# Optimization experiments

Measured on AMD Instinct MI355X. Metric: run time of the kernel, lower is better.

## Reference

```python
import jax, jax.numpy as jnp
import numpy as np


def _hausdorff(x, y):
    # x, y: [B, C, N, D] point sets per (batch, channel); rows are points.
    x2 = jnp.sum(x * x, axis=-1)                       # [B, C, N]
    y2 = jnp.sum(y * y, axis=-1)                       # [B, C, M]
    xy = jnp.einsum('bcnd,bcmd->bcnm', x, y)           # [B, C, N, M]
    d2 = x2[..., :, None] + y2[..., None, :] - 2.0 * xy
    d = jnp.sqrt(jnp.maximum(d2, 0.0))                 # Euclidean distances
    d_fwd = jnp.max(jnp.min(d, axis=-1), axis=-1)      # max_n min_m, [B, C]
    d_bwd = jnp.max(jnp.min(d, axis=-2), axis=-1)      # max_m min_n, [B, C]
    return jnp.maximum(d_fwd, d_bwd)                   # symmetric Hausdorff [B, C]


def setup_inputs() -> dict:
    key = jax.random.key(0)
    k1, k2 = jax.random.split(key)
    B, C, H, W = 8, 3, 1024, 1024
    inp = jax.random.normal(k1, (B, C, H, W), dtype=jnp.float32)
    tgt = jax.random.normal(k2, (B, C, H, W), dtype=jnp.float32)
    return {'input': inp, 'target': tgt}


def reference(input, target):
    h = _hausdorff(input, target)        # [B, C]
    # original: sum_i mean_c(h[i]) / B == mean over (B, C)
    return jnp.mean(h)
```

## Files before the change

### kernel.cpp

```cpp
#include <hip/hip_runtime.h>
#include <math.h>

constexpr int BC = 24;
constexpr int N  = 1024;
constexpr int D  = 1024;
constexpr int TILE = 128;
constexpr int SKF = 40;

typedef short short8 __attribute__((ext_vector_type(8)));
typedef float f32x4  __attribute__((ext_vector_type(4)));
typedef long lng2    __attribute__((ext_vector_type(2)));

#define FINF 3.402823466e+38f


__device__ inline unsigned pk_bf16(float a, float b) {
    unsigned ua = __float_as_uint(a) + 0x8000u;
    unsigned ub = __float_as_uint(b) + 0x8000u;
    return __builtin_amdgcn_perm(ub, ua, 0x07060302);
}

__device__ inline int pk_fp8x4(float a, float b, float c, float d) {
    int w = __builtin_amdgcn_cvt_pk_fp8_f32(a, b, 0, false);
    w = __builtin_amdgcn_cvt_pk_fp8_f32(c, d, w, true);
    return w;
}

__global__ __launch_bounds__(256) void prep_kernel(const float* __restrict__ X,
                                                   const float* __restrict__ Y,
                                                   unsigned char* __restrict__ Xf8,
                                                   unsigned char* __restrict__ Yf8,
                                                   float* __restrict__ xn,
                                                   float* __restrict__ yn) {
    int wave = threadIdx.x >> 6, lane = threadIdx.x & 63;
    int r16 = lane & 15, quad = lane >> 4;
    int wid = blockIdx.x * 4 + wave;

    float4 c0, c1, c2, c3;
    float4 n0, n1, n2, n3;

    auto src_of = [&](int st) -> const float* {
        bool isY = st >= 24576;
        int s = isY ? st - 24576 : s = st;
        s = isY ? st - 24576 : st;
        int bc = s >> 10, rkp = s & 1023;
        int R = rkp >> 4, Kp = rkp & 15;
        return (isY ? Y : X) + ((size_t)bc * N + R * 16 + r16) * D + Kp * 64 + quad * 8;
    };

    {
        const float* p = src_of(wid);
        c0 = *(const float4*)p;        c1 = *(const float4*)(p + 4);
        c2 = *(const float4*)(p + 32); c3 = *(const float4*)(p + 36);
    }
    #pragma unroll
    for (int it = 0; it < 4; it++) {
        int st = wid + it * 12288;
        if (it < 3) {
            const float* p = src_of(wid + (it + 1) * 12288);
            n0 = *(const float4*)p;        n1 = *(const float4*)(p + 4);
            n2 = *(const float4*)(p + 32); n3 = *(const float4*)(p + 36);
        }
        bool isY = st >= 24576;
        int s = isY ? st - 24576 : st;
        uint4 w;
        w.x = (unsigned)pk_fp8x4(c0.x, c0.y, c0.z, c0.w);
        w.y = (unsigned)pk_fp8x4(c1.x, c1.y, c1.z, c1.w);
        w.z = (unsigned)pk_fp8x4(c2.x, c2.y, c2.z, c2.w);
        w.w = (unsigned)pk_fp8x4(c3.x, c3.y, c3.z, c3.w);
        *(uint4*)((isY ? Yf8 : Xf8) + (size_t)s * 1024 + lane * 16) = w;

        float sm = c0.x*c0.x + c0.y*c0.y + c0.z*c0.z + c0.w*c0.w
                 + c1.x*c1.x + c1.y*c1.y + c1.z*c1.z + c1.w*c1.w
                 + c2.x*c2.x + c2.y*c2.y + c2.z*c2.z + c2.w*c2.w
                 + c3.x*c3.x + c3.y*c3.y + c3.z*c3.z + c3.w*c3.w;
        sm += __shfl_xor(sm, 16, 64);
        sm += __shfl_xor(sm, 32, 64);
        if (quad == 0) {
            int bc = s >> 10, R = (s & 1023) >> 4;
            atomicAdd(&(isY ? yn : xn)[bc * N + R * 16 + r16], sm);
        }
        c0 = n0; c1 = n1; c2 = n2; c3 = n3;
    }
}

__global__ __launch_bounds__(256, 3) void tile_f8_kernel(const unsigned char* __restrict__ Xf8,
                                                         const unsigned char* __restrict__ Yf8,
                                                         const float* __restrict__ xn,
                                                         const float* __restrict__ yn,
                                                         unsigned* __restrict__ rowmin,
                                                         unsigned* __restrict__ colmin) {
    int id = blockIdx.x;
    int bc = id >> 6;
    int tn = (id >> 3) & 7, tm = id & 7;

    int wave = threadIdx.x >> 6, lane = threadIdx.x & 63;
    int wr = wave >> 1, wc = wave & 1;
    int quad = lane >> 4, tx = lane & 15;

    const unsigned char* Xb = Xf8 + (size_t)bc * 1024 * 1024;
    const unsigned char* Yb = Yf8 + (size_t)bc * 1024 * 1024;
    const unsigned char* ax = Xb + (size_t)(tn * 8 + wr * 4) * 16 * 1024 + lane * 16;
    const unsigned char* by = Yb + (size_t)(tm * 8 + wc * 4) * 16 * 1024 + lane * 16;

    f32x4 acc[4][4];
    #pragma unroll
    for (int i = 0; i < 4; i++)
        #pragma unroll
        for (int j = 0; j < 4; j++) acc[i][j] = (f32x4)0.f;

    lng2 a[2][4], b[2][4];
    #pragma unroll
    for (int mi = 0; mi < 4; mi++) {
        a[0][mi] = *(const lng2*)(ax + mi * 16384);
        b[0][mi] = *(const lng2*)(by + mi * 16384);
    }
    #pragma unroll
    for (int Kp = 0; Kp < 16; Kp++) {
        int cur = Kp & 1, nxt = cur ^ 1;
        if (Kp < 15) {
            #pragma unroll
            for (int mi = 0; mi < 4; mi++) {
                a[nxt][mi] = *(const lng2*)(ax + mi * 16384 + (Kp + 1) * 1024);
                b[nxt][mi] = *(const lng2*)(by + mi * 16384 + (Kp + 1) * 1024);
            }
        }
        #pragma unroll
        for (int mi = 0; mi < 4; mi++)
            #pragma unroll
            for (int mj = 0; mj < 4; mj++)
                acc[mi][mj] = __builtin_amdgcn_mfma_f32_16x16x32_fp8_fp8(a[cur][mi].x, b[cur][mj].x, acc[mi][mj], 0, 0, 0);
        #pragma unroll
        for (int mi = 0; mi < 4; mi++)
            #pragma unroll
            for (int mj = 0; mj < 4; mj++)
                acc[mi][mj] = __builtin_amdgcn_mfma_f32_16x16x32_fp8_fp8(a[cur][mi].y, b[cur][mj].y, acc[mi][mj], 0, 0, 0);
    }

    int rbase = bc * N + tn * TILE + wr * 64;
    int cbase = bc * N + tm * TILE + wc * 64;
    float xnr[4][4], ynr[4];
    #pragma unroll
    for (int mi = 0; mi < 4; mi++)
        #pragma unroll
        for (int r = 0; r < 4; r++) xnr[mi][r] = xn[rbase + mi * 16 + quad * 4 + r];
    #pragma unroll
    for (int mj = 0; mj < 4; mj++) ynr[mj] = yn[cbase + mj * 16 + tx];

    float rmin[4][4], cmin[4];
    #pragma unroll
    for (int mi = 0; mi < 4; mi++)
        #pragma unroll
        for (int r = 0; r < 4; r++) rmin[mi][r] = FINF;
    #pragma unroll
    for (int mj = 0; mj < 4; mj++) cmin[mj] = FINF;

    #pragma unroll
    for (int mi = 0; mi < 4; mi++)
        #pragma unroll
        for (int mj = 0; mj < 4; mj++)
            #pragma unroll
            for (int r = 0; r < 4; r++) {
                float d2 = fmaxf(xnr[mi][r] + ynr[mj] - 2.f * acc[mi][mj][r], 0.f);
                rmin[mi][r] = fminf(rmin[mi][r], d2);
                cmin[mj]    = fminf(cmin[mj], d2);
            }

    #pragma unroll
    for (int m = 1; m < 16; m <<= 1)
        #pragma unroll
        for (int mi = 0; mi < 4; mi++)
            #pragma unroll
            for (int r = 0; r < 4; r++)
                rmin[mi][r] = fminf(rmin[mi][r], __shfl_xor(rmin[mi][r], m, 64));
    if (tx == 0) {
        #pragma unroll
        for (int mi = 0; mi < 4; mi++)
            #pragma unroll
            for (int r = 0; r < 4; r++)
                atomicMin(&rowmin[rbase + mi * 16 + quad * 4 + r], __float_as_uint(rmin[mi][r]));
    }
    #pragma unroll
    for (int m = 16; m < 64; m <<= 1)
        #pragma unroll
        for (int mj = 0; mj < 4; mj++)
            cmin[mj] = fminf(cmin[mj], __shfl_xor(cmin[mj], m, 64));
    if (quad == 0) {
        #pragma unroll
        for (int mj = 0; mj < 4; mj++)
            atomicMin(&colmin[cbase + mj * 16 + tx], __float_as_uint(cmin[mj]));
    }
}

__global__ __launch_bounds__(256) void norms_kernel(const float* __restrict__ X,
                                                    const float* __restrict__ Y,
                                                    float* __restrict__ xn,
                                                    float* __restrict__ yn) {
    int w = threadIdx.x >> 6, lane = threadIdx.x & 63;
    long rid = (long)blockIdx.x * 4 + w;
    bool isY = rid >= (long)BC * N;
    long row = isY ? rid - (long)BC * N : rid;
    const float* src = (isY ? Y : X) + row * D;
    float s = 0.f;
    #pragma unroll
    for (int q = 0; q < 4; q++) {
        float4 v = ((const float4*)src)[lane + q * 64];
        s += v.x * v.x + v.y * v.y + v.z * v.z + v.w * v.w;
    }
    #pragma unroll
    for (int m = 1; m < 64; m <<= 1) s += __shfl_xor(s, m, 64);
    if (lane == 0) (isY ? yn : xn)[row] = s;
}

__global__ __launch_bounds__(256) void tile_conv_kernel(const float* __restrict__ X,
                                                        const float* __restrict__ Y,
                                                        const float* __restrict__ xn,
                                                        const float* __restrict__ yn,
                                                        unsigned* __restrict__ rowmin,
                                                        unsigned* __restrict__ colmin) {
    __shared__ unsigned short Xs[TILE * SKF];
    __shared__ unsigned short Ys[TILE * SKF];
    int bc = blockIdx.z, tn = blockIdx.y, tm = blockIdx.x;
    const float* Xb = X + ((size_t)bc * N + (size_t)tn * TILE) * D;
    const float* Yb = Y + ((size_t)bc * N + (size_t)tm * TILE) * D;

    int t = threadIdx.x;
    int srow = t >> 3, sq = t & 7;
    int wave = t >> 6, lane = t & 63;
    int wr = wave >> 1, wc = wave & 1;
    int quad = lane >> 4, tx = lane & 15;

    f32x4 acc[4][4];
    #pragma unroll
    for (int i = 0; i < 4; i++)
        #pragma unroll
        for (int j = 0; j < 4; j++) acc[i][j] = (f32x4)0.f;

    float4 xv[4], yv[4];
    #pragma unroll
    for (int i = 0; i < 4; i++) {
        xv[i] = *(const float4*)(Xb + (size_t)(srow + i * 32) * D + sq * 4);
        yv[i] = *(const float4*)(Yb + (size_t)(srow + i * 32) * D + sq * 4);
    }

    for (int k0 = 0; k0 < D; k0 += 32) {
        __syncthreads();
        #pragma unroll
        for (int i = 0; i < 4; i++) {
            uint2 px; px.x = pk_bf16(xv[i].x, xv[i].y); px.y = pk_bf16(xv[i].z, xv[i].w);
            *(uint2*)&Xs[(srow + i * 32) * SKF + sq * 4] = px;
            uint2 py; py.x = pk_bf16(yv[i].x, yv[i].y); py.y = pk_bf16(yv[i].z, yv[i].w);
            *(uint2*)&Ys[(srow + i * 32) * SKF + sq * 4] = py;
        }
        __syncthreads();
        if (k0 + 32 < D) {
            #pragma unroll
            for (int i = 0; i < 4; i++) {
                xv[i] = *(const float4*)(Xb + (size_t)(srow + i * 32) * D + k0 + 32 + sq * 4);
                yv[i] = *(const float4*)(Yb + (size_t)(srow + i * 32) * D + k0 + 32 + sq * 4);
            }
        }
        short8 af[4], bg[4];
        #pragma unroll
        for (int mi = 0; mi < 4; mi++)
            af[mi] = *(const short8*)&Xs[(wr * 64 + mi * 16 + tx) * SKF + quad * 8];
        #pragma unroll
        for (int mj = 0; mj < 4; mj++)
            bg[mj] = *(const short8*)&Ys[(wc * 64 + mj * 16 + tx) * SKF + quad * 8];
        #pragma unroll
        for (int mi = 0; mi < 4; mi++)
            #pragma unroll
            for (int mj = 0; mj < 4; mj++)
                acc[mi][mj] = __builtin_amdgcn_mfma_f32_16x16x32_bf16(af[mi], bg[mj], acc[mi][mj], 0, 0, 0);
    }

    int rbase = bc * N + tn * TILE + wr * 64;
    int cbase = bc * N + tm * TILE + wc * 64;
    float xnr[4][4], ynr[4];
    #pragma unroll
    for (int mi = 0; mi < 4; mi++)
        #pragma unroll
        for (int r = 0; r < 4; r++) xnr[mi][r] = xn[rbase + mi * 16 + quad * 4 + r];
    #pragma unroll
    for (int mj = 0; mj < 4; mj++) ynr[mj] = yn[cbase + mj * 16 + tx];

    float rmin[4][4], cmin[4];
    #pragma unroll
    for (int mi = 0; mi < 4; mi++)
        #pragma unroll
        for (int r = 0; r < 4; r++) rmin[mi][r] = FINF;
    #pragma unroll
    for (int mj = 0; mj < 4; mj++) cmin[mj] = FINF;

    #pragma unroll
    for (int mi = 0; mi < 4; mi++)
        #pragma unroll
        for (int mj = 0; mj < 4; mj++)
            #pragma unroll
            for (int r = 0; r < 4; r++) {
                float d2 = fmaxf(xnr[mi][r] + ynr[mj] - 2.f * acc[mi][mj][r], 0.f);
                rmin[mi][r] = fminf(rmin[mi][r], d2);
                cmin[mj]    = fminf(cmin[mj], d2);
            }

    #pragma unroll
    for (int m = 1; m < 16; m <<= 1)
        #pragma unroll
        for (int mi = 0; mi < 4; mi++)
            #pragma unroll
            for (int r = 0; r < 4; r++)
                rmin[mi][r] = fminf(rmin[mi][r], __shfl_xor(rmin[mi][r], m, 64));
    if (tx == 0) {
        #pragma unroll
        for (int mi = 0; mi < 4; mi++)
            #pragma unroll
            for (int r = 0; r < 4; r++)
                atomicMin(&rowmin[rbase + mi * 16 + quad * 4 + r], __float_as_uint(rmin[mi][r]));
    }
    #pragma unroll
    for (int m = 16; m < 64; m <<= 1)
        #pragma unroll
        for (int mj = 0; mj < 4; mj++)
            cmin[mj] = fminf(cmin[mj], __shfl_xor(cmin[mj], m, 64));
    if (quad == 0) {
        #pragma unroll
        for (int mj = 0; mj < 4; mj++)
            atomicMin(&colmin[cbase + mj * 16 + tx], __float_as_uint(cmin[mj]));
    }
}

__global__ __launch_bounds__(256) void finalize_kernel(const unsigned* __restrict__ rowmin,
                                                       const unsigned* __restrict__ colmin,
                                                       float* __restrict__ out) {
    int bc = blockIdx.x;
    float v = 0.f;
    for (int i = threadIdx.x; i < N; i += 256) {
        v = fmaxf(v, __uint_as_float(rowmin[bc * N + i]));
        v = fmaxf(v, __uint_as_float(colmin[bc * N + i]));
    }
    #pragma unroll
    for (int m = 1; m < 64; m <<= 1) v = fmaxf(v, __shfl_xor(v, m, 64));
    __shared__ float ws[4];
    int lane = threadIdx.x & 63, w = threadIdx.x >> 6;
    if (lane == 0) ws[w] = v;
    __syncthreads();
    if (threadIdx.x == 0) {
        float m = fmaxf(fmaxf(ws[0], ws[1]), fmaxf(ws[2], ws[3]));
        atomicAdd(out, sqrtf(m) * (1.0f / (float)BC));
    }
}

extern "C" void kernel_launch(void* const* d_in, const int* in_sizes, int n_in,
                              void* d_out, int out_size, void* d_ws, size_t ws_size,
                              hipStream_t stream) {
    const float* X = (const float*)d_in[0];
    const float* Y = (const float*)d_in[1];
    float* out = (float*)d_out;

    unsigned* rowmin = (unsigned*)d_ws;
    unsigned* colmin = rowmin + BC * N;
    float* xn = (float*)(colmin + BC * N);
    float* yn = xn + BC * N;
    size_t head = (size_t)4 * BC * N * 4;
    size_t f8_bytes = (size_t)BC * N * D;

    hipMemsetAsync(d_ws, 0xFF, (size_t)2 * BC * N * 4, stream);
    hipMemsetAsync(xn, 0, (size_t)2 * BC * N * 4, stream);
    hipMemsetAsync(d_out, 0, sizeof(float), stream);

    if (ws_size >= head + 2 * f8_bytes) {
        unsigned char* Xf8 = (unsigned char*)d_ws + head;
        unsigned char* Yf8 = Xf8 + f8_bytes;
        prep_kernel<<<3072, 256, 0, stream>>>(X, Y, Xf8, Yf8, xn, yn);
        tile_f8_kernel<<<1536, 256, 0, stream>>>(Xf8, Yf8, xn, yn, rowmin, colmin);
    } else {
        dim3 grid(N / TILE, N / TILE, BC);
        norms_kernel<<<2 * BC * N / 4, 256, 0, stream>>>(X, Y, xn, yn);
        tile_conv_kernel<<<grid, 256, 0, stream>>>(X, Y, xn, yn, rowmin, colmin);
    }
    finalize_kernel<<<BC, 256, 0, stream>>>(rowmin, colmin, out);
}
```

Baseline: 270.0 us.

## Restructure fp8 prep kernel to whole-row waves with direct norm stores

The prep kernel now gives each wave eight full rows instead of strided 16x64 sub-tiles. Each lane reads contiguous float4s and writes fp8 bytes to the same swizzled layout through a computed inner offset. The row norm is reduced with a full-wave shuffle and stored directly, which removes the atomicAdds and the memset that zeroed the norm buffers. The grid is halved and a two-row-ahead register prefetch pipeline is used, at the cost of 4-byte scattered stores instead of 16-byte stores.

New measurement: 287.2 us. 6.4% more time.

```diff
diff --git a/kernel.cpp b/kernel.cpp
--- a/kernel.cpp
+++ b/kernel.cpp
@@ -33,54 +33,44 @@
                                                    float* __restrict__ xn,
                                                    float* __restrict__ yn) {
     int wave = threadIdx.x >> 6, lane = threadIdx.x & 63;
-    int r16 = lane & 15, quad = lane >> 4;
-    int wid = blockIdx.x * 4 + wave;
-
-    float4 c0, c1, c2, c3;
-    float4 n0, n1, n2, n3;
-
-    auto src_of = [&](int st) -> const float* {
-        bool isY = st >= 24576;
-        int s = isY ? st - 24576 : s = st;
-        s = isY ? st - 24576 : st;
-        int bc = s >> 10, rkp = s & 1023;
-        int R = rkp >> 4, Kp = rkp & 15;
-        return (isY ? Y : X) + ((size_t)bc * N + R * 16 + r16) * D + Kp * 64 + quad * 8;
-    };
-
-    {
-        const float* p = src_of(wid);
-        c0 = *(const float4*)p;        c1 = *(const float4*)(p + 4);
-        c2 = *(const float4*)(p + 32); c3 = *(const float4*)(p + 36);
-    }
-    #pragma unroll
-    for (int it = 0; it < 4; it++) {
-        int st = wid + it * 12288;
-        if (it < 3) {
-            const float* p = src_of(wid + (it + 1) * 12288);
-            n0 = *(const float4*)p;        n1 = *(const float4*)(p + 4);
-            n2 = *(const float4*)(p + 32); n3 = *(const float4*)(p + 36);
-        }
-        bool isY = st >= 24576;
-        int s = isY ? st - 24576 : st;
-        uint4 w;
-        w.x = (unsigned)pk_fp8x4(c0.x, c0.y, c0.z, c0.w);
-        w.y = (unsigned)pk_fp8x4(c1.x, c1.y, c1.z, c1.w);
-        w.z = (unsigned)pk_fp8x4(c2.x, c2.y, c2.z, c2.w);
-        w.w = (unsigned)pk_fp8x4(c3.x, c3.y, c3.z, c3.w);
-        *(uint4*)((isY ? Yf8 : Xf8) + (size_t)s * 1024 + lane * 16) = w;
-
-        float sm = c0.x*c0.x + c0.y*c0.y + c0.z*c0.z + c0.w*c0.w
-                 + c1.x*c1.x + c1.y*c1.y + c1.z*c1.z + c1.w*c1.w
-                 + c2.x*c2.x + c2.y*c2.y + c2.z*c2.z + c2.w*c2.w
-                 + c3.x*c3.x + c3.y*c3.y + c3.z*c3.z + c3.w*c3.w;
-        sm += __shfl_xor(sm, 16, 64);
-        sm += __shfl_xor(sm, 32, 64);
-        if (quad == 0) {
-            int bc = s >> 10, R = (s & 1023) >> 4;
-            atomicAdd(&(isY ? yn : xn)[bc * N + R * 16 + r16], sm);
-        }
-        c0 = n0; c1 = n1; c2 = n2; c3 = n3;
+    int rid0 = (blockIdx.x * 4 + wave) * 8;
+    bool isY = rid0 >= 24576;
+    int row0 = isY ? rid0 - 24576 : rid0;
+    const float* __restrict__ src = (isY ? Y : X) + (size_t)row0 * D + lane * 4;
+    unsigned char* __restrict__ dst = isY ? Yf8 : Xf8;
+    float* __restrict__ nrm = isY ? yn : xn;
+
+    int KpL   = lane >> 4;
+    int inner = (((lane >> 1) & 3) << 8) | (((lane >> 3) & 1) << 3) | ((lane & 1) << 2);
+    unsigned char* dbase = dst + (size_t)((row0 & ~15) + KpL) * 1024
+                               + (row0 & 15) * 16 + inner;
+
+    float4 A[4], Bv[4], Cv[4];
+    #pragma unroll
+    for (int q = 0; q < 4; q++) A[q]  = *(const float4*)(src + q * 256);
+    #pragma unroll
+    for (int q = 0; q < 4; q++) Bv[q] = *(const float4*)(src + D + q * 256);
+
+    #pragma unroll
+    for (int r = 0; r < 8; r++) {
+        if (r < 6) {
+            #pragma unroll
+            for (int q = 0; q < 4; q++)
+                Cv[q] = *(const float4*)(src + (size_t)(r + 2) * D + q * 256);
+        }
+        float s = 0.f;
+        #pragma unroll
+        for (int q = 0; q < 4; q++) {
+            unsigned w = (unsigned)pk_fp8x4(A[q].x, A[q].y, A[q].z, A[q].w);
+            *(unsigned*)(dbase + q * 4096 + r * 16) = w;
+            s += A[q].x * A[q].x + A[q].y * A[q].y
+               + A[q].z * A[q].z + A[q].w * A[q].w;
+        }
+        #pragma unroll
+        for (int m = 1; m < 64; m <<= 1) s += __shfl_xor(s, m, 64);
+        if (lane == 0) nrm[row0 + r] = s;
+        #pragma unroll
+        for (int q = 0; q < 4; q++) { A[q] = Bv[q]; Bv[q] = Cv[q]; }
     }
 }
 
@@ -365,13 +355,12 @@
     size_t f8_bytes = (size_t)BC * N * D;
 
     hipMemsetAsync(d_ws, 0xFF, (size_t)2 * BC * N * 4, stream);
-    hipMemsetAsync(xn, 0, (size_t)2 * BC * N * 4, stream);
     hipMemsetAsync(d_out, 0, sizeof(float), stream);
 
     if (ws_size >= head + 2 * f8_bytes) {
         unsigned char* Xf8 = (unsigned char*)d_ws + head;
         unsigned char* Yf8 = Xf8 + f8_bytes;
-        prep_kernel<<<3072, 256, 0, stream>>>(X, Y, Xf8, Yf8, xn, yn);
+        prep_kernel<<<1536, 256, 0, stream>>>(X, Y, Xf8, Yf8, xn, yn);
         tile_f8_kernel<<<1536, 256, 0, stream>>>(Xf8, Yf8, xn, yn, rowmin, colmin);
     } else {
         dim3 grid(N / TILE, N / TILE, BC);
```
